# Optimization experiments

Hardware: AMD Instinct MI355X
Metric: run time of the kernel (lower is better)

## Reference

```python
import jax, jax.numpy as jnp
import numpy as np

EMB = 768
HEADS = 12
HEAD_DIM = EMB // HEADS


def setup_inputs() -> dict:
    key = jax.random.key(0)
    ks = jax.random.split(key, 9)
    B, L, D = 4, 2048, EMB
    s = 1.0 / np.sqrt(D)
    return {
        "x": jax.random.normal(ks[0], (B, L, D), dtype=jnp.float32),
        "Wq": jax.random.normal(ks[1], (D, D), dtype=jnp.float32) * s,
        "bq": jnp.zeros((D,), dtype=jnp.float32),
        "Wk": jax.random.normal(ks[2], (D, D), dtype=jnp.float32) * s,
        "bk": jnp.zeros((D,), dtype=jnp.float32),
        "Wv": jax.random.normal(ks[3], (D, D), dtype=jnp.float32) * s,
        "bv": jnp.zeros((D,), dtype=jnp.float32),
        "Wo": jax.random.normal(ks[4], (D, D), dtype=jnp.float32) * s,
        "bo": jnp.zeros((D,), dtype=jnp.float32),
    }


def reference(x, Wq, bq, Wk, bk, Wv, bv, Wo, bo):
    B, L, D = x.shape
    H, hd = HEADS, HEAD_DIM
    # QKV projections -> [B, H, L, hd]
    def proj(W, b):
        return (x @ W + b).reshape(B, L, H, hd).transpose(0, 2, 1, 3)
    Q = proj(Wq, bq)
    K = proj(Wk, bk)
    V = proj(Wv, bv)
    # scores [B, H, L, L]
    scores = jnp.einsum("bhqd,bhkd->bhqk", Q, K) / jnp.sqrt(jnp.float32(hd))
    attn = jax.nn.softmax(scores, axis=-1)
    out = jnp.einsum("bhqk,bhkd->bhqd", attn, V)  # [B,H,L,hd]
    out = out.transpose(0, 2, 1, 3).reshape(B, L, D)
    return out @ Wo + bo
```

## Files before the change

### kernel.cpp

```cpp
#include <hip/hip_runtime.h>
#include <math.h>

#define TL 2048
#define TD 768
#define NH 12
#define HD 64
#define NB 4
#define MTOT (NB * TL)

typedef __bf16 bf16;
typedef __attribute__((ext_vector_type(4))) __bf16 bf16x4;
typedef __attribute__((ext_vector_type(8))) __bf16 bf16x8;
typedef __attribute__((ext_vector_type(4))) float floatx4;

#define QSCALE 0.18033688011112042f

#define MFMA16(A, B, C) __builtin_amdgcn_mfma_f32_16x16x32_bf16(A, B, C, 0, 0, 0)

__device__ __forceinline__ void gl_lds16(const void* g, void* l) {
    __builtin_amdgcn_global_load_lds(
        (const __attribute__((address_space(1))) void*)g,
        (__attribute__((address_space(3))) void*)l, 16, 0, 0);
}

__device__ __forceinline__ floatx4 exp2x4(floatx4 a) {
    floatx4 r;
    r.x = __builtin_amdgcn_exp2f(a.x);
    r.y = __builtin_amdgcn_exp2f(a.y);
    r.z = __builtin_amdgcn_exp2f(a.z);
    r.w = __builtin_amdgcn_exp2f(a.w);
    return r;
}

__device__ __forceinline__ int kperm_inv(int r) {
    return (r & 35) | (((r >> 2) & 3) << 3) | (((r >> 4) & 1) << 2);
}
__device__ __forceinline__ int kinv128(int r) {
    return (r & 64) | kperm_inv(r & 63);
}

__global__ __launch_bounds__(256)
void prep_kernel(const float* __restrict__ x,
                 const float* __restrict__ W0, const float* __restrict__ W1,
                 const float* __restrict__ W2, const float* __restrict__ W3,
                 bf16* __restrict__ xb,
                 bf16* __restrict__ T0, bf16* __restrict__ T1,
                 bf16* __restrict__ T2, bf16* __restrict__ T3)
{
    __shared__ float Ts[64][65];
    const int bid = blockIdx.x;
    const int t = threadIdx.x;
    if (bid < 576) {
        const int z = bid / 144, rem = bid % 144;
        const float* W = z == 0 ? W0 : z == 1 ? W1 : z == 2 ? W2 : W3;
        bf16*       T = z == 0 ? T0 : z == 1 ? T1 : z == 2 ? T2 : T3;
        const int k0 = (rem / 12) * 64, n0 = (rem % 12) * 64;
        const int rr = t >> 4, cc = (t & 15) * 4;
#pragma unroll
        for (int i = 0; i < 4; ++i) {
            int row = rr + i * 16;
            float4 v = *(const float4*)(W + (size_t)(k0 + row) * TD + n0 + cc);
            Ts[row][cc] = v.x; Ts[row][cc + 1] = v.y;
            Ts[row][cc + 2] = v.z; Ts[row][cc + 3] = v.w;
        }
        __syncthreads();
#pragma unroll
        for (int i = 0; i < 4; ++i) {
            int n = rr + i * 16;
            bf16x4 pk;
#pragma unroll
            for (int j = 0; j < 4; ++j) pk[j] = (bf16)Ts[cc + j][n];
            *(bf16x4*)(T + (size_t)(n0 + n) * TD + k0 + cc) = pk;
        }
    } else {
        size_t i = ((size_t)(bid - 576) * 256 + t) * 4;
        float4 v = *(const float4*)(x + i);
        bf16x4 o;
        o[0] = (bf16)v.x; o[1] = (bf16)v.y; o[2] = (bf16)v.z; o[3] = (bf16)v.w;
        *(bf16x4*)(xb + i) = o;
    }
}

__global__ __launch_bounds__(256)
void qkv_gemm(const bf16* __restrict__ xb,
              const bf16* __restrict__ Wqt, const bf16* __restrict__ Wkt,
              const bf16* __restrict__ Wvt,
              const float* __restrict__ bq, const float* __restrict__ bk,
              const float* __restrict__ bv,
              bf16* __restrict__ Q, bf16* __restrict__ K, bf16* __restrict__ Vt)
{
    __shared__ __align__(16) bf16 As[128 * 64];
    __shared__ __align__(16) bf16 Bs[128 * 64];
    __shared__ __align__(16) bf16 Eb[4][16 * 72];

    const int t = threadIdx.x;
    const int lane = t & 63, w = t >> 6;
    const int quad = lane >> 4, l16 = lane & 15;
    const int m0 = blockIdx.x * 128;
    const int n0 = blockIdx.y * 128;
    const int which = blockIdx.z;
    const bf16*  W    = which == 0 ? Wqt : which == 1 ? Wkt : Wvt;
    const float* bias = which == 0 ? bq  : which == 1 ? bk  : bv;
    const float scale = which == 0 ? QSCALE : 1.0f;

    const int rm = (w >> 1) * 64, cn = (w & 1) * 64;

    floatx4 acc[4][4];
#pragma unroll
    for (int i = 0; i < 4; ++i)
#pragma unroll
        for (int j = 0; j < 4; ++j) acc[i][j] = (floatx4){0.f, 0.f, 0.f, 0.f};

    const bf16* gA[4];
    const bf16* gB[4];
#pragma unroll
    for (int i = 0; i < 4; ++i) {
        int n = t + i * 256, r = n >> 3, s = ((n & 7) ^ (r & 7)) * 8;
        gA[i] = xb + (size_t)(m0 + r) * TD + s;
        gB[i] = W + (size_t)(n0 + r) * TD + s;
    }

    for (int kk = 0; kk < TD; kk += 64) {
#pragma unroll
        for (int i = 0; i < 4; ++i) {
            gl_lds16(gA[i] + kk, As + t * 8 + i * 2048);
            gl_lds16(gB[i] + kk, Bs + t * 8 + i * 2048);
        }
        __syncthreads();
#pragma unroll
        for (int ks = 0; ks < 2; ++ks) {
            bf16x8 af[4], bfr[4];
#pragma unroll
            for (int mb = 0; mb < 4; ++mb) {
                int r = rm + mb * 16 + l16;
                af[mb] = *(const bf16x8*)&As[r * 64 + (((ks * 4 + quad) ^ (r & 7)) * 8)];
            }
#pragma unroll
            for (int nb = 0; nb < 4; ++nb) {
                int r = cn + nb * 16 + l16;
                bfr[nb] = *(const bf16x8*)&Bs[r * 64 + (((ks * 4 + quad) ^ (r & 7)) * 8)];
            }
#pragma unroll
            for (int mb = 0; mb < 4; ++mb)
#pragma unroll
                for (int nb = 0; nb < 4; ++nb)
                    acc[mb][nb] = MFMA16(af[mb], bfr[nb], acc[mb][nb]);
        }
        __syncthreads();
    }

    float bsc[4];
#pragma unroll
    for (int nb = 0; nb < 4; ++nb)
        bsc[nb] = bias[n0 + cn + nb * 16 + l16] * scale;

    const int token0 = m0 + rm;
    const int b  = token0 >> 11;
    const int l0 = token0 & (TL - 1);
    const int h  = (n0 + cn) >> 6;
    const int bh = b * NH + h;
    bf16* Ew = Eb[w];

    if (which < 2) {
        bf16* gp = (which == 0 ? Q : K) + ((size_t)bh * TL + l0) * HD;
#pragma unroll
        for (int mb = 0; mb < 4; ++mb) {
#pragma unroll
            for (int nb = 0; nb < 4; ++nb)
#pragma unroll
                for (int r = 0; r < 4; ++r)
                    Ew[(quad * 4 + r) * 72 + nb * 16 + l16] =
                        (bf16)(acc[mb][nb][r] * scale + bsc[nb]);
#pragma unroll
            for (int i = 0; i < 2; ++i) {
                int row = i * 8 + (lane >> 3), seg = lane & 7;
                bf16x8 v = *(const bf16x8*)&Ew[row * 72 + seg * 8];
                *(bf16x8*)(gp + (size_t)(mb * 16 + row) * HD + seg * 8) = v;
            }
        }
    } else {
#pragma unroll
        for (int nb = 0; nb < 4; ++nb) {
#pragma unroll
            for (int mb = 0; mb < 4; ++mb) {
                bf16x4 pk;
#pragma unroll
                for (int r = 0; r < 4; ++r) pk[r] = (bf16)(acc[mb][nb][r] + bsc[nb]);
                *(bf16x4*)&Ew[l16 * 72 + mb * 16 + quad * 4] = pk;
            }
#pragma unroll
            for (int i = 0; i < 2; ++i) {
                int row = i * 8 + (lane >> 3), seg = lane & 7;
                bf16x8 v = *(const bf16x8*)&Ew[row * 72 + seg * 8];
                *(bf16x8*)(Vt + ((size_t)bh * HD + nb * 16 + row) * TL + l0 + seg * 8) = v;
            }
        }
    }
}

__global__ __launch_bounds__(256)
void attn_kernel(const bf16* __restrict__ Q, const bf16* __restrict__ K,
                 const bf16* __restrict__ Vt, bf16* __restrict__ O)
{
    __shared__ __align__(16) bf16 Ks[128 * 64];
    __shared__ __align__(16) bf16 Vs[64 * 128];

    const int t = threadIdx.x;
    const int lane = t & 63, w = t >> 6;
    const int quad = lane >> 4, l16 = lane & 15;

    const int n = blockIdx.y * gridDim.x + blockIdx.x;
    const int xcd = n & 7, s = n >> 3;
    const int bh = xcd * 6 + (s >> 4);
    const int q0 = (s & 15) * 128;

    const bf16* Qb = Q + (size_t)bh * TL * HD;
    const bf16* Kb = K + (size_t)bh * TL * HD;
    const bf16* Vb = Vt + (size_t)bh * HD * TL;

    const int qw = q0 + w * 32;
    bf16x8 qf[2][2];
#pragma unroll
    for (int mb = 0; mb < 2; ++mb)
#pragma unroll
        for (int ks = 0; ks < 2; ++ks)
            qf[mb][ks] = *(const bf16x8*)(Qb + (size_t)(qw + mb * 16 + l16) * HD
                                          + ks * 32 + quad * 8);

    float lrow[2] = {0.f, 0.f};
    floatx4 o[2][4];
#pragma unroll
    for (int mb = 0; mb < 2; ++mb)
#pragma unroll
        for (int db = 0; db < 4; ++db) o[mb][db] = (floatx4){0.f, 0.f, 0.f, 0.f};

    const bf16* gK[4];
    const bf16* gV[4];
#pragma unroll
    for (int i = 0; i < 4; ++i) {
        int nk = t + i * 256;
        int rk = nk >> 3, sk = ((nk & 7) ^ (rk & 7)) * 8;
        gK[i] = Kb + (size_t)kinv128(rk) * HD + sk;
        int rv = nk >> 4, sv = ((nk & 15) ^ (rv & 15)) * 8;
        gV[i] = Vb + (size_t)rv * TL + sv;
    }

    for (int kt = 0; kt < TL / 128; ++kt) {
        const int k0 = kt * 128;
        __syncthreads();
#pragma unroll
        for (int i = 0; i < 4; ++i) {
            gl_lds16(gK[i] + (size_t)k0 * HD, Ks + (t + i * 256) * 8);
            gl_lds16(gV[i] + k0,              Vs + (t + i * 256) * 8);
        }
        __syncthreads();

#pragma unroll
        for (int ks = 0; ks < 4; ++ks) {
            floatx4 s2[2][2];
#pragma unroll
            for (int nbp = 0; nbp < 2; ++nbp) {
                int rr = (ks * 2 + nbp) * 16 + l16;
                bf16x8 kf0 = *(const bf16x8*)&Ks[rr * 64 + ((quad ^ (rr & 7)) * 8)];
                bf16x8 kf1 = *(const bf16x8*)&Ks[rr * 64 + (((4 + quad) ^ (rr & 7)) * 8)];
#pragma unroll
                for (int mb = 0; mb < 2; ++mb) {
                    floatx4 a = (floatx4){0.f, 0.f, 0.f, 0.f};
                    a = MFMA16(kf0, qf[mb][0], a);
                    a = MFMA16(kf1, qf[mb][1], a);
                    s2[mb][nbp] = a;
                }
            }
            bf16x8 pA[2];
#pragma unroll
            for (int mb = 0; mb < 2; ++mb) {
                floatx4 p0 = exp2x4(s2[mb][0]);
                floatx4 p1 = exp2x4(s2[mb][1]);
                lrow[mb] += (p0.x + p0.y + p0.z + p0.w) + (p1.x + p1.y + p1.z + p1.w);
                bf16x8 pk;
                pk[0] = (bf16)p0.x; pk[1] = (bf16)p0.y; pk[2] = (bf16)p0.z; pk[3] = (bf16)p0.w;
                pk[4] = (bf16)p1.x; pk[5] = (bf16)p1.y; pk[6] = (bf16)p1.z; pk[7] = (bf16)p1.w;
                pA[mb] = pk;
            }
#pragma unroll
            for (int db = 0; db < 4; ++db) {
                int rr = db * 16 + l16;
                int slot = rr * 16 + ((ks * 4 + quad) ^ (rr & 15));
                bf16x8 vf = *(const bf16x8*)&Vs[slot * 8];
#pragma unroll
                for (int mb = 0; mb < 2; ++mb)
                    o[mb][db] = MFMA16(pA[mb], vf, o[mb][db]);
            }
        }
    }

    const int b = bh / NH, h = bh % NH;
#pragma unroll
    for (int mb = 0; mb < 2; ++mb) {
        lrow[mb] += __shfl_xor(lrow[mb], 16);
        lrow[mb] += __shfl_xor(lrow[mb], 32);
        floatx4 inv;
#pragma unroll
        for (int r = 0; r < 4; ++r)
            inv[r] = 1.0f / __shfl(lrow[mb], (lane & 48) | (quad * 4 + r));
#pragma unroll
        for (int db = 0; db < 4; ++db)
#pragma unroll
            for (int r = 0; r < 4; ++r) {
                int l = qw + mb * 16 + quad * 4 + r;
                O[((size_t)b * TL + l) * TD + h * HD + db * 16 + l16] =
                    (bf16)(o[mb][db][r] * inv[r]);
            }
    }
}

__global__ __launch_bounds__(256)
void oproj_gemm(const bf16* __restrict__ A, const bf16* __restrict__ Wt,
                const float* __restrict__ bo, float* __restrict__ out)
{
    __shared__ __align__(16) bf16 As[128 * 64];
    __shared__ __align__(16) bf16 Bs[64 * 64];
    __shared__ __align__(16) float Ef[4][16 * 36];

    const int t = threadIdx.x;
    const int lane = t & 63, w = t >> 6;
    const int quad = lane >> 4, l16 = lane & 15;
    const int m0 = blockIdx.x * 128;
    const int n0 = blockIdx.y * 64;
    const int rm = (w >> 1) * 64, cn = (w & 1) * 32;

    floatx4 acc[4][2];
#pragma unroll
    for (int i = 0; i < 4; ++i)
#pragma unroll
        for (int j = 0; j < 2; ++j) acc[i][j] = (floatx4){0.f, 0.f, 0.f, 0.f};

    const bf16* gA[4];
    const bf16* gB[2];
#pragma unroll
    for (int i = 0; i < 4; ++i) {
        int nn = t + i * 256, r = nn >> 3, s = ((nn & 7) ^ (r & 7)) * 8;
        gA[i] = A + (size_t)(m0 + r) * TD + s;
    }
#pragma unroll
    for (int i = 0; i < 2; ++i) {
        int nn = t + i * 256, r = nn >> 3, s = ((nn & 7) ^ (r & 7)) * 8;
        gB[i] = Wt + (size_t)(n0 + r) * TD + s;
    }

    for (int kk = 0; kk < TD; kk += 64) {
#pragma unroll
        for (int i = 0; i < 4; ++i)
            gl_lds16(gA[i] + kk, As + (t + i * 256) * 8);
#pragma unroll
        for (int i = 0; i < 2; ++i)
            gl_lds16(gB[i] + kk, Bs + (t + i * 256) * 8);
        __syncthreads();
#pragma unroll
        for (int ks = 0; ks < 2; ++ks) {
            bf16x8 af[4], bfr[2];
#pragma unroll
            for (int mb = 0; mb < 4; ++mb) {
                int r = rm + mb * 16 + l16;
                af[mb] = *(const bf16x8*)&As[r * 64 + (((ks * 4 + quad) ^ (r & 7)) * 8)];
            }
#pragma unroll
            for (int nb = 0; nb < 2; ++nb) {
                int r = cn + nb * 16 + l16;
                bfr[nb] = *(const bf16x8*)&Bs[r * 64 + (((ks * 4 + quad) ^ (r & 7)) * 8)];
            }
#pragma unroll
            for (int mb = 0; mb < 4; ++mb)
#pragma unroll
                for (int nb = 0; nb < 2; ++nb)
                    acc[mb][nb] = MFMA16(af[mb], bfr[nb], acc[mb][nb]);
        }
        __syncthreads();
    }

    float bb[2];
#pragma unroll
    for (int nb = 0; nb < 2; ++nb) bb[nb] = bo[n0 + cn + nb * 16 + l16];

    float* Ew = Ef[w];
#pragma unroll
    for (int mb = 0; mb < 4; ++mb) {
#pragma unroll
        for (int nb = 0; nb < 2; ++nb)
#pragma unroll
            for (int r = 0; r < 4; ++r)
                Ew[(quad * 4 + r) * 36 + nb * 16 + l16] = acc[mb][nb][r] + bb[nb];
#pragma unroll
        for (int i = 0; i < 2; ++i) {
            int row = i * 8 + (lane >> 3), seg = lane & 7;
            float4 v = *(const float4*)&Ew[row * 36 + seg * 4];
            *(float4*)(out + (size_t)(m0 + rm + mb * 16 + row) * TD + n0 + cn + seg * 4) = v;
        }
    }
}

extern "C" void kernel_launch(void* const* d_in, const int* in_sizes, int n_in,
                              void* d_out, int out_size, void* d_ws, size_t ws_size,
                              hipStream_t stream)
{
    const float* x  = (const float*)d_in[0];
    const float* Wq = (const float*)d_in[1];
    const float* bq = (const float*)d_in[2];
    const float* Wk = (const float*)d_in[3];
    const float* bk = (const float*)d_in[4];
    const float* Wv = (const float*)d_in[5];
    const float* bv = (const float*)d_in[6];
    const float* Wo = (const float*)d_in[7];
    const float* bo = (const float*)d_in[8];

    const size_t NXE = (size_t)MTOT * TD;
    const size_t NWE = (size_t)TD * TD;

    bf16* xb  = (bf16*)d_ws;
    bf16* Wqt = xb + NXE;
    bf16* Wkt = Wqt + NWE;
    bf16* Wvt = Wkt + NWE;
    bf16* Wot = Wvt + NWE;
    bf16* Qb  = Wot + NWE;
    bf16* Kb  = Qb + NXE;
    bf16* Vtb = Kb + NXE;
    bf16* Ob  = Vtb + NXE;

    prep_kernel<<<576 + 6144, 256, 0, stream>>>(x, Wq, Wk, Wv, Wo,
                                                xb, Wqt, Wkt, Wvt, Wot);
    qkv_gemm<<<dim3(MTOT / 128, TD / 128, 3), 256, 0, stream>>>(
        xb, Wqt, Wkt, Wvt, bq, bk, bv, Qb, Kb, Vtb);
    attn_kernel<<<dim3(TL / 128, NB * NH), 256, 0, stream>>>(Qb, Kb, Vtb, Ob);
    oproj_gemm<<<dim3(MTOT / 128, TD / 64), 256, 0, stream>>>(Ob, Wot, bo,
                                                              (float*)d_out);
}
```

Baseline: 218.8 us.

## Load V fragments directly from global in attention, shrink LDS tiles, reuse LDS for epilogues

The attention kernel now streams 64-key tiles instead of 128. It stages only K through LDS and reads V^T fragments straight from global memory into registers, which cuts LDS use per block and may raise occupancy. The QKV and output-projection GEMMs drop their separate epilogue staging buffers and reuse the A tile's LDS. The QKV GEMM also gets a launch-bounds occupancy hint. The cost is that V now comes through uncoalesced-ish global loads with latency exposed before the barrier, and the loop runs twice as many iterations with extra synchronisation.

```diff
diff --git a/kernel.cpp b/kernel.cpp
--- a/kernel.cpp
+++ b/kernel.cpp
@@ -34,9 +34,6 @@
 
 __device__ __forceinline__ int kperm_inv(int r) {
     return (r & 35) | (((r >> 2) & 3) << 3) | (((r >> 4) & 1) << 2);
-}
-__device__ __forceinline__ int kinv128(int r) {
-    return (r & 64) | kperm_inv(r & 63);
 }
 
 __global__ __launch_bounds__(256)
@@ -81,7 +78,7 @@
     }
 }
 
-__global__ __launch_bounds__(256)
+__global__ __launch_bounds__(256, 4)
 void qkv_gemm(const bf16* __restrict__ xb,
               const bf16* __restrict__ Wqt, const bf16* __restrict__ Wkt,
               const bf16* __restrict__ Wvt,
@@ -91,7 +88,6 @@
 {
     __shared__ __align__(16) bf16 As[128 * 64];
     __shared__ __align__(16) bf16 Bs[128 * 64];
-    __shared__ __align__(16) bf16 Eb[4][16 * 72];
 
     const int t = threadIdx.x;
     const int lane = t & 63, w = t >> 6;
@@ -159,7 +155,7 @@
     const int l0 = token0 & (TL - 1);
     const int h  = (n0 + cn) >> 6;
     const int bh = b * NH + h;
-    bf16* Ew = Eb[w];
+    bf16* Ew = As + w * (16 * 72);
 
     if (which < 2) {
         bf16* gp = (which == 0 ? Q : K) + ((size_t)bh * TL + l0) * HD;
@@ -202,8 +198,7 @@
 void attn_kernel(const bf16* __restrict__ Q, const bf16* __restrict__ K,
                  const bf16* __restrict__ Vt, bf16* __restrict__ O)
 {
-    __shared__ __align__(16) bf16 Ks[128 * 64];
-    __shared__ __align__(16) bf16 Vs[64 * 128];
+    __shared__ __align__(16) bf16 Ks[64 * 64];
 
     const int t = threadIdx.x;
     const int lane = t & 63, w = t >> 6;
@@ -234,64 +229,68 @@
 #pragma unroll
         for (int db = 0; db < 4; ++db) o[mb][db] = (floatx4){0.f, 0.f, 0.f, 0.f};
 
-    const bf16* gK[4];
-    const bf16* gV[4];
-#pragma unroll
-    for (int i = 0; i < 4; ++i) {
-        int nk = t + i * 256;
-        int rk = nk >> 3, sk = ((nk & 7) ^ (rk & 7)) * 8;
-        gK[i] = Kb + (size_t)kinv128(rk) * HD + sk;
-        int rv = nk >> 4, sv = ((nk & 15) ^ (rv & 15)) * 8;
-        gV[i] = Vb + (size_t)rv * TL + sv;
-    }
-
-    for (int kt = 0; kt < TL / 128; ++kt) {
-        const int k0 = kt * 128;
-        __syncthreads();
-#pragma unroll
-        for (int i = 0; i < 4; ++i) {
-            gl_lds16(gK[i] + (size_t)k0 * HD, Ks + (t + i * 256) * 8);
-            gl_lds16(gV[i] + k0,              Vs + (t + i * 256) * 8);
-        }
-        __syncthreads();
-
-#pragma unroll
-        for (int ks = 0; ks < 4; ++ks) {
-            floatx4 s2[2][2];
-#pragma unroll
-            for (int nbp = 0; nbp < 2; ++nbp) {
-                int rr = (ks * 2 + nbp) * 16 + l16;
-                bf16x8 kf0 = *(const bf16x8*)&Ks[rr * 64 + ((quad ^ (rr & 7)) * 8)];
-                bf16x8 kf1 = *(const bf16x8*)&Ks[rr * 64 + (((4 + quad) ^ (rr & 7)) * 8)];
-#pragma unroll
-                for (int mb = 0; mb < 2; ++mb) {
-                    floatx4 a = (floatx4){0.f, 0.f, 0.f, 0.f};
-                    a = MFMA16(kf0, qf[mb][0], a);
-                    a = MFMA16(kf1, qf[mb][1], a);
-                    s2[mb][nbp] = a;
-                }
-            }
-            bf16x8 pA[2];
+    const bf16* gK[2];
+#pragma unroll
+    for (int i = 0; i < 2; ++i) {
+        int nn = t + i * 256, r = nn >> 3, sg = ((nn & 7) ^ (r & 7)) * 8;
+        gK[i] = Kb + (size_t)kperm_inv(r) * HD + sg;
+    }
+
+    const bf16* vp[4];
+#pragma unroll
+    for (int db = 0; db < 4; ++db)
+        vp[db] = Vb + (size_t)(db * 16 + l16) * TL + quad * 8;
+
+    for (int kt = 0; kt < TL / 64; ++kt) {
+        const int k0 = kt * 64;
+        __syncthreads();
+        gl_lds16(gK[0] + (size_t)k0 * HD, Ks + t * 8);
+        gl_lds16(gK[1] + (size_t)k0 * HD, Ks + (t + 256) * 8);
+        bf16x8 vf[2][4];
+#pragma unroll
+        for (int ks = 0; ks < 2; ++ks)
+#pragma unroll
+            for (int db = 0; db < 4; ++db)
+                vf[ks][db] = *(const bf16x8*)(vp[db] + k0 + ks * 32);
+        __syncthreads();
+
+        floatx4 s2[2][4];
+#pragma unroll
+        for (int nb = 0; nb < 4; ++nb) {
+            int r = nb * 16 + l16;
+            bf16x8 kf0 = *(const bf16x8*)&Ks[r * 64 + ((quad ^ (r & 7)) * 8)];
+            bf16x8 kf1 = *(const bf16x8*)&Ks[r * 64 + (((4 + quad) ^ (r & 7)) * 8)];
 #pragma unroll
             for (int mb = 0; mb < 2; ++mb) {
-                floatx4 p0 = exp2x4(s2[mb][0]);
-                floatx4 p1 = exp2x4(s2[mb][1]);
+                floatx4 a = (floatx4){0.f, 0.f, 0.f, 0.f};
+                a = MFMA16(kf0, qf[mb][0], a);
+                a = MFMA16(kf1, qf[mb][1], a);
+                s2[mb][nb] = a;
+            }
+        }
+
+        bf16x8 pA[2][2];
+#pragma unroll
+        for (int mb = 0; mb < 2; ++mb) {
+#pragma unroll
+            for (int ks = 0; ks < 2; ++ks) {
+                floatx4 p0 = exp2x4(s2[mb][2 * ks]);
+                floatx4 p1 = exp2x4(s2[mb][2 * ks + 1]);
                 lrow[mb] += (p0.x + p0.y + p0.z + p0.w) + (p1.x + p1.y + p1.z + p1.w);
                 bf16x8 pk;
                 pk[0] = (bf16)p0.x; pk[1] = (bf16)p0.y; pk[2] = (bf16)p0.z; pk[3] = (bf16)p0.w;
                 pk[4] = (bf16)p1.x; pk[5] = (bf16)p1.y; pk[6] = (bf16)p1.z; pk[7] = (bf16)p1.w;
-                pA[mb] = pk;
-            }
-#pragma unroll
-            for (int db = 0; db < 4; ++db) {
-                int rr = db * 16 + l16;
-                int slot = rr * 16 + ((ks * 4 + quad) ^ (rr & 15));
-                bf16x8 vf = *(const bf16x8*)&Vs[slot * 8];
+                pA[mb][ks] = pk;
+            }
+        }
+
+#pragma unroll
+        for (int ks = 0; ks < 2; ++ks)
+#pragma unroll
+            for (int db = 0; db < 4; ++db)
 #pragma unroll
                 for (int mb = 0; mb < 2; ++mb)
-                    o[mb][db] = MFMA16(pA[mb], vf, o[mb][db]);
-            }
-        }
+                    o[mb][db] = MFMA16(pA[mb][ks], vf[ks][db], o[mb][db]);
     }
 
     const int b = bh / NH, h = bh % NH;
@@ -320,7 +319,6 @@
 {
     __shared__ __align__(16) bf16 As[128 * 64];
     __shared__ __align__(16) bf16 Bs[64 * 64];
-    __shared__ __align__(16) float Ef[4][16 * 36];
 
     const int t = threadIdx.x;
     const int lane = t & 63, w = t >> 6;
@@ -382,7 +380,7 @@
 #pragma unroll
     for (int nb = 0; nb < 2; ++nb) bb[nb] = bo[n0 + cn + nb * 16 + l16];
 
-    float* Ew = Ef[w];
+    float* Ew = (float*)As + w * (16 * 36);
 #pragma unroll
     for (int mb = 0; mb < 4; ++mb) {
 #pragma unroll
```

New measurement: 279.4 us. 1.28x slower.
